# Kernel optimization log

Hardware: AMD Instinct MI355X
Metric: run time of the kernel (lower is better)

## Reference

```python
import jax, jax.numpy as jnp
import numpy as np

CUTOFFS = (2000, 20000, 50000)  # shortlist end, tail cluster boundaries; last == vocab
B, H, V = 8192, 1024, 50000
N_TAIL = len(CUTOFFS) - 1  # 2


def setup_inputs() -> dict:
    key = jax.random.key(0)
    ks = jax.random.split(key, 10)
    hidden = jax.random.normal(ks[0], (B, H), jnp.float32)
    targets = jax.random.randint(ks[1], (B,), 0, V, dtype=jnp.int64)
    embed_weight = jax.random.normal(ks[2], (V, H), jnp.float32) * 0.02
    # head: tail_vectors = nn.Linear(H, n_tail) -> W:(n_tail,H), b:(n_tail,)
    tail_vec_W = jax.random.normal(ks[3], (N_TAIL, H), jnp.float32) * 0.02
    tail_vec_b = jax.random.normal(ks[4], (N_TAIL,), jnp.float32) * 0.02
    shortlist_bias = jax.random.normal(ks[5], (CUTOFFS[0],), jnp.float32)
    bias0 = jax.random.normal(ks[6], (CUTOFFS[1] - CUTOFFS[0],), jnp.float32)
    bias1 = jax.random.normal(ks[7], (CUTOFFS[2] - CUTOFFS[1],), jnp.float32)
    # down_i = nn.Linear(H, H // 4**i, bias=False) -> W:(H//4**i, H)
    down0_W = jax.random.normal(ks[8], (H, H), jnp.float32) * (1.0 / np.sqrt(H))
    down1_W = jax.random.normal(ks[9], (H // 4, H), jnp.float32) * (1.0 / np.sqrt(H))
    return {
        "hidden": hidden, "embed_weight": embed_weight,
        "tail_vec_W": tail_vec_W, "tail_vec_b": tail_vec_b,
        "shortlist_bias": shortlist_bias, "bias0": bias0, "bias1": bias1,
        "down0_W": down0_W, "down1_W": down1_W, "targets": targets,
    }


def _cluster_ids(targets):
    # data-dependent sizes -> host-side index computation (matches torch nonzero)
    t = np.asarray(targets)
    ids = []
    for i in range(N_TAIL):
        ids.append(jnp.asarray(np.nonzero((t >= CUTOFFS[i]) & (t < CUTOFFS[i + 1]))[0]))
    return ids


def reference(hidden, embed_weight, tail_vec_W, tail_vec_b, shortlist_bias,
              bias0, bias1, down0_W, down1_W, targets):
    idx0, idx1 = _cluster_ids(targets)
    # head: shortlist logits + one logit per tail cluster
    shortlist = embed_weight[:CUTOFFS[0]]                       # (c0, H)
    head = jnp.concatenate(
        [hidden @ shortlist.T + shortlist_bias[None, :],         # (B, c0)
         hidden @ tail_vec_W.T + tail_vec_b[None, :]], axis=1)   # (B, n_tail)
    # tail cluster 0: down0 is H->H (reduce_factor**0 == 1, still applied)
    dec0 = embed_weight[CUTOFFS[0]:CUTOFFS[1]] @ down0_W.T       # (18000, H)
    out0 = (hidden[idx0] @ down0_W.T) @ dec0.T + bias0[None, :]  # (n0, 18000)
    # tail cluster 1: down1 is H -> H//4
    dec1 = embed_weight[CUTOFFS[1]:CUTOFFS[2]] @ down1_W.T       # (30000, 256)
    out1 = (hidden[idx1] @ down1_W.T) @ dec1.T + bias1[None, :]  # (n1, 30000)
    return (head, out0, out1)
```

## Files before the change

kernel.cpp:

```cpp
#include <hip/hip_runtime.h>
#include <hip/hip_bf16.h>

#define CUT0 2000
#define CUT1 20000
#define CUT2 50000
#define BSZ  8192
#define HDIM 1024
#define N0MAX 18000
#define N1MAX 30000
#define HEADW 2002

typedef __attribute__((ext_vector_type(8))) short bf16x8;
typedef __attribute__((ext_vector_type(4))) float f32x4;
typedef __attribute__((ext_vector_type(4))) unsigned short us4;

__device__ __forceinline__ unsigned short f2bf(float x) {
    unsigned u = __float_as_uint(x);
    unsigned r = u + 0x7fffu + ((u >> 16) & 1u);
    return (unsigned short)(r >> 16);
}

__device__ __forceinline__ bf16x8 pack8(f32x4 a, f32x4 b) {
    bf16x8 w;
    w[0] = (short)f2bf(a[0]); w[1] = (short)f2bf(a[1]);
    w[2] = (short)f2bf(a[2]); w[3] = (short)f2bf(a[3]);
    w[4] = (short)f2bf(b[0]); w[5] = (short)f2bf(b[1]);
    w[6] = (short)f2bf(b[2]); w[7] = (short)f2bf(b[3]);
    return w;
}

typedef const __attribute__((address_space(1))) void* gas_ptr;
typedef __attribute__((address_space(3))) void* las_ptr;

__device__ __forceinline__ void load_lds16(const void* g, void* l) {
    __builtin_amdgcn_global_load_lds((gas_ptr)g, (las_ptr)l, 16, 0, 0);
}

#define CVT_NBLK 1643
__global__ __launch_bounds__(256) void cvt_all(
    const float* __restrict__ embed,  const float* __restrict__ tailW,
    const float* __restrict__ down0,  const float* __restrict__ down1,
    const float* __restrict__ slbias, const float* __restrict__ tailb,
    const int* __restrict__ targets,
    unsigned short* __restrict__ ebf,
    unsigned short* __restrict__ d0bf, unsigned short* __restrict__ d1bf,
    float* __restrict__ bias2002,
    int* __restrict__ n0p, int* __restrict__ n1p,
    int* __restrict__ idx0, int* __restrict__ idx1)
{
    const int b = blockIdx.x;
    if (b == 1642) {
        __shared__ int s0[256], s1[256];
        const int t = threadIdx.x;
        const int base = t * 32;
        int tg[32];
        int c0n = 0, c1n = 0;
#pragma unroll
        for (int i = 0; i < 32; ++i) {
            tg[i] = targets[base + i];
            c0n += (tg[i] >= CUT0 && tg[i] < CUT1) ? 1 : 0;
            c1n += (tg[i] >= CUT1) ? 1 : 0;
        }
        s0[t] = c0n; s1[t] = c1n;
        __syncthreads();
        for (int o = 1; o < 256; o <<= 1) {
            int v0 = 0, v1 = 0;
            if (t >= o) { v0 = s0[t - o]; v1 = s1[t - o]; }
            __syncthreads();
            s0[t] += v0; s1[t] += v1;
            __syncthreads();
        }
        int p0 = s0[t] - c0n, p1 = s1[t] - c1n;
#pragma unroll
        for (int i = 0; i < 32; ++i) {
            if (tg[i] >= CUT0 && tg[i] < CUT1)      idx0[p0++] = base + i;
            else if (tg[i] >= CUT1)                 idx1[p1++] = base + i;
        }
        if (t == 255) { *n0p = s0[255]; *n1p = s1[255]; }
        return;
    }
    if (b == 1641) {
        for (int j = threadIdx.x; j < HEADW; j += 256)
            bias2002[j] = (j < CUT0) ? slbias[j] : tailb[j - CUT0];
        return;
    }
    const float* src; unsigned short* dst; long long e;
    if (b < 1000)      { src = embed; dst = ebf;  e = (long long)b * 2048; }
    else if (b == 1000){ src = tailW; dst = ebf + (size_t)CUT0 * HDIM; e = 0; }
    else if (b < 1513) { src = down0; dst = d0bf; e = (long long)(b - 1001) * 2048; }
    else               { src = down1; dst = d1bf; e = (long long)(b - 1513) * 2048; }
    const long long i = e + (long long)threadIdx.x * 8;
    f32x4 a = *(const f32x4*)(src + i);
    f32x4 c = *(const f32x4*)(src + i + 4);
    us4 p = { f2bf(a[0]), f2bf(a[1]), f2bf(a[2]), f2bf(a[3]) };
    us4 q = { f2bf(c[0]), f2bf(c[1]), f2bf(c[2]), f2bf(c[3]) };
    *(us4*)(dst + i)     = p;
    *(us4*)(dst + i + 4) = q;
}

template<bool A_F32, bool SPLIT_GATHER, bool OUT_BF16, bool HAS_BIAS>
__device__ __forceinline__ void gemm_body(
    unsigned short (* __restrict__ As)[8192],
    unsigned short (* __restrict__ Bs)[8192],
    const void* __restrict__ Av, const float* __restrict__ AgF,
    const unsigned short* __restrict__ B,
    int gsplit, int gbase, const int* __restrict__ idxTail,
    int M, int N, int K,
    const float* __restrict__ bias,
    void* __restrict__ Cv, long long cbase, int ldC,
    int m0, int n0)
{
    const int tid  = threadIdx.x;
    const int wave = tid >> 6, lane = tid & 63;
    const int wr = wave >> 2;
    const int wc = wave & 3;
    const int lrow = lane & 15;
    const int quad = lane >> 4;

    const int srow = lane >> 2;
    const int scol = (((lane & 3) ^ ((srow >> 1) & 3)) << 3);
    int tr0 = wave * 32 + srow, tr1 = tr0 + 16;
    int bn0 = n0 + tr0; bn0 = bn0 < N ? bn0 : N - 1;
    int bn1 = n0 + tr1; bn1 = bn1 < N ? bn1 : N - 1;
    const unsigned short* bP0 = B + (long long)bn0 * K + scol;
    const unsigned short* bP1 = B + (long long)bn1 * K + scol;

    const unsigned short* aP0 = nullptr;
    const unsigned short* aP1 = nullptr;
    const float* aF = nullptr;
    int oA0 = 0, oA1 = 0, sA0 = 0, sA1 = 0;
    if constexpr (!A_F32) {
        int am0 = m0 + tr0; am0 = am0 < M ? am0 : M - 1;
        int am1 = m0 + tr1; am1 = am1 < M ? am1 : M - 1;
        long long ar0, ar1;
        if constexpr (SPLIT_GATHER) {
            ar0 = (am0 < gsplit) ? (long long)(gbase + am0) : (long long)idxTail[am0 - gsplit];
            ar1 = (am1 < gsplit) ? (long long)(gbase + am1) : (long long)idxTail[am1 - gsplit];
        } else { ar0 = am0; ar1 = am1; }
        const unsigned short* Ab = (const unsigned short*)Av;
        aP0 = Ab + ar0 * (long long)K + scol;
        aP1 = Ab + ar1 * (long long)K + scol;
    } else {
        const int rA  = lane >> 1;
        const int trA = wave * 32 + rA;
        int amF = m0 + trA; amF = amF < M ? amF : M - 1;
        long long rowi; const float* bp;
        if constexpr (SPLIT_GATHER) {
            if (amF < gsplit) { rowi = (long long)(gbase + amF); bp = (const float*)Av; }
            else              { rowi = (long long)idxTail[amF - gsplit]; bp = AgF; }
        } else { rowi = amF; bp = (const float*)Av; }
        aF  = bp + rowi * (long long)K;
        sA0 = (lane & 1);
        sA1 = 2 + (lane & 1);
        const int xA = (rA >> 1) & 3;
        oA0 = trA * 32 + ((sA0 ^ xA) << 3);
        oA1 = trA * 32 + ((sA1 ^ xA) << 3);
    }

    f32x4 acc[8][4];
#pragma unroll
    for (int i = 0; i < 8; ++i)
#pragma unroll
        for (int j = 0; j < 4; ++j) acc[i][j] = (f32x4){0.f, 0.f, 0.f, 0.f};

    const int KT = K >> 5;

    auto issueB = [&](int tt) {
        unsigned short* bs = &Bs[tt & 3][wave * 1024];
        load_lds16(bP0 + (tt << 5), bs);
        load_lds16(bP1 + (tt << 5), bs + 512);
    };
    auto issueA16 = [&](int tt) {
        unsigned short* as = &As[tt & 3][wave * 1024];
        load_lds16(aP0 + (tt << 5), as);
        load_lds16(aP1 + (tt << 5), as + 512);
    };

    const int npro = KT < 3 ? KT : 3;
    for (int tt = 0; tt < npro; ++tt) {
        if constexpr (!A_F32) {
            issueB(tt);
            issueA16(tt);
        } else {
            const float* p = aF + (tt << 5);
            f32x4 x0 = *(const f32x4*)(p + sA0 * 8);
            f32x4 x1 = *(const f32x4*)(p + sA0 * 8 + 4);
            f32x4 y0 = *(const f32x4*)(p + sA1 * 8);
            f32x4 y1 = *(const f32x4*)(p + sA1 * 8 + 4);
            issueB(tt);
            *(bf16x8*)&As[tt & 3][oA0] = pack8(x0, x1);
            *(bf16x8*)&As[tt & 3][oA1] = pack8(y0, y1);
        }
    }
    if constexpr (A_F32)
        asm volatile("s_waitcnt lgkmcnt(0)" ::: "memory");

    const int rdswz = ((quad ^ ((lrow >> 1) & 3)) << 3);

    for (int t = 0; t < KT; ++t) {
        const int tt = t + 3;
        const bool pf = (tt < KT);

        f32x4 x0, x1, y0, y1;
        if constexpr (!A_F32) {
            if (pf) { issueB(tt); issueA16(tt); }
        } else {
            if (pf) {
                const float* p = aF + (tt << 5);
                x0 = *(const f32x4*)(p + sA0 * 8);
                x1 = *(const f32x4*)(p + sA0 * 8 + 4);
                y0 = *(const f32x4*)(p + sA1 * 8);
                y1 = *(const f32x4*)(p + sA1 * 8 + 4);
                issueB(tt);
            }
        }

        int infl = KT - 1 - t; if (infl > 3) infl = 3;
        if constexpr (!A_F32) {
            if (infl >= 3)      asm volatile("s_waitcnt vmcnt(12)" ::: "memory");
            else if (infl == 2) asm volatile("s_waitcnt vmcnt(8)"  ::: "memory");
            else if (infl == 1) asm volatile("s_waitcnt vmcnt(4)"  ::: "memory");
            else                asm volatile("s_waitcnt vmcnt(0)"  ::: "memory");
        } else {
            if (infl >= 3)      asm volatile("s_waitcnt vmcnt(8)"  ::: "memory");
            else if (infl == 2) asm volatile("s_waitcnt vmcnt(4)"  ::: "memory");
            else if (infl == 1) asm volatile("s_waitcnt vmcnt(2)"  ::: "memory");
            else                asm volatile("s_waitcnt vmcnt(0)"  ::: "memory");
        }

        __builtin_amdgcn_s_barrier();
        asm volatile("" ::: "memory");

        const unsigned short* Asl = &As[t & 3][0];
        const unsigned short* Bsl = &Bs[t & 3][0];

        bf16x8 a[8], b[4];
#pragma unroll
        for (int mi = 0; mi < 8; ++mi) {
            const int R = wr * 128 + mi * 16 + lrow;
            a[mi] = *(const bf16x8*)&Asl[R * 32 + rdswz];
        }
#pragma unroll
        for (int nj = 0; nj < 4; ++nj) {
            const int R = wc * 64 + nj * 16 + lrow;
            b[nj] = *(const bf16x8*)&Bsl[R * 32 + rdswz];
        }

        __builtin_amdgcn_s_setprio(1);
#pragma unroll
        for (int mi = 0; mi < 8; ++mi)
#pragma unroll
            for (int nj = 0; nj < 4; ++nj)
                acc[mi][nj] = __builtin_amdgcn_mfma_f32_16x16x32_bf16(
                    a[mi], b[nj], acc[mi][nj], 0, 0, 0);
        __builtin_amdgcn_s_setprio(0);

        if constexpr (A_F32) {
            if (pf) {
                *(bf16x8*)&As[tt & 3][oA0] = pack8(x0, x1);
                *(bf16x8*)&As[tt & 3][oA1] = pack8(y0, y1);
            }
            asm volatile("s_waitcnt lgkmcnt(0)" ::: "memory");
        }

        asm volatile("" ::: "memory");
        __builtin_amdgcn_s_barrier();
    }

#pragma unroll
    for (int mi = 0; mi < 8; ++mi) {
#pragma unroll
        for (int v = 0; v < 4; ++v) {
            int m = m0 + wr * 128 + mi * 16 + quad * 4 + v;
            if (m >= M) continue;
#pragma unroll
            for (int nj = 0; nj < 4; ++nj) {
                int n = n0 + wc * 64 + nj * 16 + lrow;
                if (n >= N) continue;
                float r = acc[mi][nj][v];
                if constexpr (OUT_BF16) {
                    ((unsigned short*)Cv)[(long long)m * ldC + n] = f2bf(r);
                } else {
                    if constexpr (HAS_BIAS) r += bias[n];
                    ((float*)Cv)[cbase + (long long)m * ldC + n] = r;
                }
            }
        }
    }
}

__global__ __launch_bounds__(512) void gemm_mid(
    const float* __restrict__ hidden, const float* __restrict__ embed,
    const unsigned short* __restrict__ ebf,
    const unsigned short* __restrict__ d0bf, const unsigned short* __restrict__ d1bf,
    const float* __restrict__ bias2002,
    const int* __restrict__ idx0, const int* __restrict__ idx1,
    const int* __restrict__ n0p, const int* __restrict__ n1p,
    float* __restrict__ out,
    unsigned short* __restrict__ c0, unsigned short* __restrict__ c1)
{
    __shared__ unsigned short As[4][8192];
    __shared__ unsigned short Bs[4][8192];
    int id = (int)(((long long)blockIdx.x * 405) % 818);
    if (id < 256) {
        const int bx = id & 7, by = id >> 3;
        gemm_body<true, false, false, true>(
            As, Bs, hidden, nullptr, ebf, 0, 0, nullptr,
            BSZ, HEADW, HDIM, bias2002, out, 0ll, HEADW,
            by * 256, bx * 256);
        return;
    }
    id -= 256;
    if (id < 4 * 103) {
        const int bx = id & 3, by = id >> 2;
        const int M = N0MAX + *n0p;
        const int m0 = by * 256;
        if (m0 >= M) return;
        gemm_body<true, true, true, false>(
            As, Bs, embed, hidden, d0bf, N0MAX, CUT0, idx0,
            M, HDIM, HDIM, nullptr, c0, 0ll, HDIM, m0, bx * 256);
        return;
    }
    id -= 412;
    const int M = N1MAX + *n1p;
    const int m0 = id * 256;
    if (m0 >= M) return;
    gemm_body<true, true, true, false>(
        As, Bs, embed, hidden, d1bf, N1MAX, CUT1, idx1,
        M, 256, HDIM, nullptr, c1, 0ll, 256, m0, 0);
}

__global__ __launch_bounds__(512) void gemm_out01(
    const unsigned short* __restrict__ c0, const unsigned short* __restrict__ c1,
    const int* __restrict__ n0p, const int* __restrict__ n1p,
    const float* __restrict__ bias0, const float* __restrict__ bias1,
    float* __restrict__ out)
{
    __shared__ unsigned short As[4][8192];
    __shared__ unsigned short Bs[4][8192];
    int bx = blockIdx.x;
    const unsigned short *A, *B; const float* bias;
    int M, N, K, ldC; long long cbase;
    if (bx < 71) {
        A = c0 + (size_t)N0MAX * HDIM; B = c0; bias = bias0;
        M = *n0p; N = N0MAX; K = HDIM; ldC = N0MAX;
        cbase = (long long)BSZ * HEADW;
    } else {
        bx -= 71;
        A = c1 + (size_t)N1MAX * 256; B = c1; bias = bias1;
        M = *n1p; N = N1MAX; K = 256; ldC = N1MAX;
        cbase = (long long)BSZ * HEADW + (long long)(*n0p) * N0MAX;
    }
    const int m0 = (int)blockIdx.y * 256;
    const int n0 = bx * 256;
    if (m0 >= M) return;
    gemm_body<false, false, false, true>(
        As, Bs, A, nullptr, B, 0, 0, nullptr,
        M, N, K, bias, out, cbase, ldC, m0, n0);
}

extern "C" void kernel_launch(void* const* d_in, const int* in_sizes, int n_in,
                              void* d_out, int out_size, void* d_ws, size_t ws_size,
                              hipStream_t stream) {
    (void)in_sizes; (void)n_in; (void)out_size; (void)ws_size;
    const float* hidden  = (const float*)d_in[0];
    const float* embed   = (const float*)d_in[1];
    const float* tailW   = (const float*)d_in[2];
    const float* tailb   = (const float*)d_in[3];
    const float* slbias  = (const float*)d_in[4];
    const float* bias0   = (const float*)d_in[5];
    const float* bias1   = (const float*)d_in[6];
    const float* down0   = (const float*)d_in[7];
    const float* down1   = (const float*)d_in[8];
    const int*   targets = (const int*)d_in[9];
    float* out = (float*)d_out;

    char* ws = (char*)d_ws;
    int* n0p  = (int*)ws;
    int* n1p  = n0p + 1;
    int* idx0 = (int*)(ws + 256);
    int* idx1 = idx0 + BSZ;
    size_t off = 256 + 2 * (size_t)BSZ * 4;
    unsigned short* ebf  = (unsigned short*)(ws + off); off += (size_t)HEADW * HDIM * 2;
    float* bias2002      = (float*)(ws + off);          off += 2048 * 4;
    unsigned short* c0   = (unsigned short*)(ws + off);
    off += (size_t)(N0MAX + BSZ) * HDIM * 2;
    unsigned short* c1   = (unsigned short*)(ws + off);
    off += (size_t)(N1MAX + BSZ) * 256 * 2;
    unsigned short* d0bf = (unsigned short*)(ws + off); off += (size_t)HDIM * HDIM * 2;
    unsigned short* d1bf = (unsigned short*)(ws + off); off += (size_t)256 * HDIM * 2;

    cvt_all<<<CVT_NBLK, 256, 0, stream>>>(
        embed, tailW, down0, down1, slbias, tailb, targets,
        ebf, d0bf, d1bf, bias2002, n0p, n1p, idx0, idx1);

    gemm_mid<<<818, 512, 0, stream>>>(
        hidden, embed, ebf, d0bf, d1bf, bias2002,
        idx0, idx1, n0p, n1p, out, c0, c1);

    gemm_out01<<<dim3(189, 32), 512, 0, stream>>>(
        c0, c1, n0p, n1p, bias0, bias1, out);
}
```

Before: 1.575 ms.

## Shrink output GEMM LDS ring to double buffer and remove block-id shuffle

Makes the shared-memory ring depth a template parameter and drops the output GEMM kernel to a 2-stage ring (64KB LDS instead of 128KB), adding launch_bounds min-blocks hint to raise occupancy. The mid GEMM keeps its 4-stage ring but replaces the modular block-id permutation with a plain linear mapping. Trades prefetch depth for more resident blocks per CU; the shallower pipeline may expose more memory latency and the linear mapping changes load balance across CUs.

```diff
diff --git a/kernel.cpp b/kernel.cpp
--- a/kernel.cpp
+++ b/kernel.cpp
@@ -98,7 +98,7 @@
     *(us4*)(dst + i + 4) = q;
 }
 
-template<bool A_F32, bool SPLIT_GATHER, bool OUT_BF16, bool HAS_BIAS>
+template<int RING, bool A_F32, bool SPLIT_GATHER, bool OUT_BF16, bool HAS_BIAS>
 __device__ __forceinline__ void gemm_body(
     unsigned short (* __restrict__ As)[8192],
     unsigned short (* __restrict__ Bs)[8192],
@@ -110,6 +110,10 @@
     void* __restrict__ Cv, long long cbase, int ldC,
     int m0, int n0)
 {
+    static_assert(RING == 2 || RING == 4, "ring size");
+    constexpr int PF = RING - 1;
+    constexpr int SMSK = RING - 1;
+
     const int tid  = threadIdx.x;
     const int wave = tid >> 6, lane = tid & 63;
     const int wr = wave >> 2;
@@ -166,17 +170,17 @@
     const int KT = K >> 5;
 
     auto issueB = [&](int tt) {
-        unsigned short* bs = &Bs[tt & 3][wave * 1024];
+        unsigned short* bs = &Bs[tt & SMSK][wave * 1024];
         load_lds16(bP0 + (tt << 5), bs);
         load_lds16(bP1 + (tt << 5), bs + 512);
     };
     auto issueA16 = [&](int tt) {
-        unsigned short* as = &As[tt & 3][wave * 1024];
+        unsigned short* as = &As[tt & SMSK][wave * 1024];
         load_lds16(aP0 + (tt << 5), as);
         load_lds16(aP1 + (tt << 5), as + 512);
     };
 
-    const int npro = KT < 3 ? KT : 3;
+    const int npro = KT < PF ? KT : PF;
     for (int tt = 0; tt < npro; ++tt) {
         if constexpr (!A_F32) {
             issueB(tt);
@@ -188,8 +192,8 @@
             f32x4 y0 = *(const f32x4*)(p + sA1 * 8);
             f32x4 y1 = *(const f32x4*)(p + sA1 * 8 + 4);
             issueB(tt);
-            *(bf16x8*)&As[tt & 3][oA0] = pack8(x0, x1);
-            *(bf16x8*)&As[tt & 3][oA1] = pack8(y0, y1);
+            *(bf16x8*)&As[tt & SMSK][oA0] = pack8(x0, x1);
+            *(bf16x8*)&As[tt & SMSK][oA1] = pack8(y0, y1);
         }
     }
     if constexpr (A_F32)
@@ -198,7 +202,7 @@
     const int rdswz = ((quad ^ ((lrow >> 1) & 3)) << 3);
 
     for (int t = 0; t < KT; ++t) {
-        const int tt = t + 3;
+        const int tt = t + PF;
         const bool pf = (tt < KT);
 
         f32x4 x0, x1, y0, y1;
@@ -215,7 +219,7 @@
             }
         }
 
-        int infl = KT - 1 - t; if (infl > 3) infl = 3;
+        int infl = KT - 1 - t; if (infl > PF) infl = PF;
         if constexpr (!A_F32) {
             if (infl >= 3)      asm volatile("s_waitcnt vmcnt(12)" ::: "memory");
             else if (infl == 2) asm volatile("s_waitcnt vmcnt(8)"  ::: "memory");
@@ -231,8 +235,8 @@
         __builtin_amdgcn_s_barrier();
         asm volatile("" ::: "memory");
 
-        const unsigned short* Asl = &As[t & 3][0];
-        const unsigned short* Bsl = &Bs[t & 3][0];
+        const unsigned short* Asl = &As[t & SMSK][0];
+        const unsigned short* Bsl = &Bs[t & SMSK][0];
 
         bf16x8 a[8], b[4];
 #pragma unroll
@@ -257,8 +261,8 @@
 
         if constexpr (A_F32) {
             if (pf) {
-                *(bf16x8*)&As[tt & 3][oA0] = pack8(x0, x1);
-                *(bf16x8*)&As[tt & 3][oA1] = pack8(y0, y1);
+                *(bf16x8*)&As[tt & SMSK][oA0] = pack8(x0, x1);
+                *(bf16x8*)&As[tt & SMSK][oA1] = pack8(y0, y1);
             }
             asm volatile("s_waitcnt lgkmcnt(0)" ::: "memory");
         }
@@ -301,10 +305,10 @@
 {
     __shared__ unsigned short As[4][8192];
     __shared__ unsigned short Bs[4][8192];
-    int id = (int)(((long long)blockIdx.x * 405) % 818);
+    int id = blockIdx.x;
     if (id < 256) {
         const int bx = id & 7, by = id >> 3;
-        gemm_body<true, false, false, true>(
+        gemm_body<4, true, false, false, true>(
             As, Bs, hidden, nullptr, ebf, 0, 0, nullptr,
             BSZ, HEADW, HDIM, bias2002, out, 0ll, HEADW,
             by * 256, bx * 256);
@@ -316,7 +320,7 @@
         const int M = N0MAX + *n0p;
         const int m0 = by * 256;
         if (m0 >= M) return;
-        gemm_body<true, true, true, false>(
+        gemm_body<4, true, true, true, false>(
             As, Bs, embed, hidden, d0bf, N0MAX, CUT0, idx0,
             M, HDIM, HDIM, nullptr, c0, 0ll, HDIM, m0, bx * 256);
         return;
@@ -325,19 +329,19 @@
     const int M = N1MAX + *n1p;
     const int m0 = id * 256;
     if (m0 >= M) return;
-    gemm_body<true, true, true, false>(
+    gemm_body<4, true, true, true, false>(
         As, Bs, embed, hidden, d1bf, N1MAX, CUT1, idx1,
         M, 256, HDIM, nullptr, c1, 0ll, 256, m0, 0);
 }
 
-__global__ __launch_bounds__(512) void gemm_out01(
+__global__ __launch_bounds__(512, 4) void gemm_out01(
     const unsigned short* __restrict__ c0, const unsigned short* __restrict__ c1,
     const int* __restrict__ n0p, const int* __restrict__ n1p,
     const float* __restrict__ bias0, const float* __restrict__ bias1,
     float* __restrict__ out)
 {
-    __shared__ unsigned short As[4][8192];
-    __shared__ unsigned short Bs[4][8192];
+    __shared__ unsigned short As[2][8192];
+    __shared__ unsigned short Bs[2][8192];
     int bx = blockIdx.x;
     const unsigned short *A, *B; const float* bias;
     int M, N, K, ldC; long long cbase;
@@ -354,7 +358,7 @@
     const int m0 = (int)blockIdx.y * 256;
     const int n0 = bx * 256;
     if (m0 >= M) return;
-    gemm_body<false, false, false, true>(
+    gemm_body<2, false, false, false, true>(
         As, Bs, A, nullptr, B, 0, 0, nullptr,
         M, N, K, bias, out, cbase, ldC, m0, n0);
 }
```

Result: slower. 3.178 ms (+101.7%).
